# Kernel optimization log

Measured on AMD Instinct MI355X. Metric: run time of the kernel, lower is better.

The kernel has to match this reference:

```python
import jax, jax.numpy as jnp
import numpy as np

N_HEADS = 16
ATT_DIM = 1024
HEAD_DIM = ATT_DIM // N_HEADS
SCALE = 1.0 / (HEAD_DIM ** 0.5)


def setup_inputs() -> dict:
    key = jax.random.key(0)
    k1, k2 = jax.random.split(key)
    B, N, D = 4, 2048, 1024
    X = jax.random.normal(k1, (B, N, D), dtype=jnp.float32)
    W_qkv = jax.random.normal(k2, (3 * ATT_DIM, D), dtype=jnp.float32) * 0.02  # trunc_normal-ish std
    return {"X": X, "W_qkv": W_qkv}


def reference(X, W_qkv):
    B, N, D = X.shape
    # qkv projection (bias=False): X @ W^T -> [b, n, 3*att_dim]
    QKV = jnp.einsum('bnd,od->bno', X, W_qkv)
    # rearrange 'b n (p h d) -> p b h n d'
    QKV = QKV.reshape(B, N, 3, N_HEADS, HEAD_DIM).transpose(2, 0, 3, 1, 4)
    Q, K, V = QKV[0], QKV[1], QKV[2]
    # scaled dot-product attention, full NxN scores (as in source)
    scores = jnp.einsum('bhid,bhjd->bhij', Q, K) * SCALE
    S = jax.nn.softmax(scores, axis=-1)
    # dropout rate is 0.0 -> identity
    Y = jnp.einsum('bhij,bhjd->bhid', S, V)
    # 'b h n d -> b n (h d)'; out_proj is Identity (out_dim == att_dim)
    return Y.transpose(0, 2, 1, 3).reshape(B, N, N_HEADS * HEAD_DIM)
```

## Files before the change

### kernel.cpp

```cpp
#include <hip/hip_runtime.h>

#define BATCH   4
#define SEQ     2048
#define DMODEL  1024
#define NHEADS  16
#define HDIM    64
#define QSC     0.18033688f

typedef short s16x8 __attribute__((ext_vector_type(8)));
typedef float f32x4 __attribute__((ext_vector_type(4)));
typedef const __attribute__((address_space(1))) unsigned int* gas_t;
typedef __attribute__((address_space(3))) unsigned int* las_t;

__device__ inline unsigned short f2bf(float f) {
    unsigned int u = __float_as_uint(f);
    u += 0x7FFF + ((u >> 16) & 1);
    return (unsigned short)(u >> 16);
}

__device__ __forceinline__ float exp2_fast(float x) {
#if __has_builtin(__builtin_amdgcn_exp2f)
    return __builtin_amdgcn_exp2f(x);
#else
    return exp2f(x);
#endif
}

__device__ __forceinline__ float rcp_fast(float x) {
#if __has_builtin(__builtin_amdgcn_rcpf)
    return __builtin_amdgcn_rcpf(x);
#else
    return 1.0f / x;
#endif
}

__device__ __forceinline__ unsigned int pack_bf16x2(float lo, float hi) {
    unsigned int a = __float_as_uint(lo) + 0x8000u;
    unsigned int b = __float_as_uint(hi) + 0x8000u;
#if __has_builtin(__builtin_amdgcn_perm)
    return __builtin_amdgcn_perm(b, a, 0x07060302u);
#else
    return (a >> 16) | (b & 0xFFFF0000u);
#endif
}

__global__ void cvt_bf16(const float* __restrict__ in,
                         unsigned short* __restrict__ out, int n4) {
    int i = blockIdx.x * blockDim.x + threadIdx.x;
    if (i >= n4) return;
    float4 v = ((const float4*)in)[i];
    ushort4 o;
    o.x = f2bf(v.x); o.y = f2bf(v.y); o.z = f2bf(v.z); o.w = f2bf(v.w);
    ((ushort4*)out)[i] = o;
}

__global__ __launch_bounds__(256, 4) void qkv_gemm(
    const unsigned short* __restrict__ Xb,
    const unsigned short* __restrict__ Wb,
    unsigned short* __restrict__ Qo,
    unsigned short* __restrict__ Ko,
    unsigned short* __restrict__ Vt)
{
    __shared__ __align__(16) unsigned short As[2][128 * 32];
    __shared__ __align__(16) unsigned short Bs[2][128 * 32];

    const int t    = threadIdx.x;
    const int m0   = blockIdx.y * 128;
    const int n0   = blockIdx.x * 128;
    const int wid  = t >> 6;
    const int lane = t & 63;
    const int l15  = lane & 15;
    const int quad = lane >> 4;
    const int wm   = (wid >> 1) * 64;
    const int wn   = (wid & 1) * 64;

    const int srow = t >> 1;
    const int koff = (t & 1) * 16;

    const unsigned short* gA = &Xb[(size_t)(m0 + srow) * 1024 + koff];
    const unsigned short* gB = &Wb[(size_t)(n0 + srow) * 1024 + koff];

    f32x4 acc[4][4] = {};
    uint4 ra0, ra1, rb0, rb1;

    auto gload = [&](int k0) {
        const uint4* pa = (const uint4*)(gA + k0);
        ra0 = pa[0]; ra1 = pa[1];
        const uint4* pb = (const uint4*)(gB + k0);
        rb0 = pb[0]; rb1 = pb[1];
    };
    auto swrite = [&](int buf) {
        uint4* sa = (uint4*)&As[buf][srow * 32 + koff];
        sa[0] = ra0; sa[1] = ra1;
        uint4* sb = (uint4*)&Bs[buf][srow * 32 + koff];
        sb[0] = rb0; sb[1] = rb1;
    };

    gload(0);
    swrite(0);
    __syncthreads();

    int cur = 0;
    #pragma unroll 1
    for (int k0 = 0; k0 < 1024; k0 += 32) {
        const bool more = (k0 + 32) < 1024;
        if (more) gload(k0 + 32);

        s16x8 af[4], bf[4];
        #pragma unroll
        for (int mt = 0; mt < 4; mt++)
            af[mt] = *(const s16x8*)&As[cur][(wm + mt * 16 + l15) * 32 + quad * 8];
        #pragma unroll
        for (int nt = 0; nt < 4; nt++)
            bf[nt] = *(const s16x8*)&Bs[cur][(wn + nt * 16 + l15) * 32 + quad * 8];
        #pragma unroll
        for (int mt = 0; mt < 4; mt++)
            #pragma unroll
            for (int nt = 0; nt < 4; nt++)
                acc[mt][nt] = __builtin_amdgcn_mfma_f32_16x16x32_bf16(
                    af[mt], bf[nt], acc[mt][nt], 0, 0, 0);

        if (more) swrite(cur ^ 1);
        __syncthreads();
        cur ^= 1;
    }

    #pragma unroll
    for (int mt = 0; mt < 4; mt++) {
        const int mbase = m0 + wm + mt * 16 + quad * 4;
        #pragma unroll
        for (int nt = 0; nt < 4; nt++) {
            const int o  = n0 + wn + nt * 16 + l15;
            const int p  = o >> 10;
            const int oo = o & 1023;
            const int h  = oo >> 6;
            const int d  = oo & 63;
            #pragma unroll
            for (int r = 0; r < 4; r++) {
                const int mm = mbase + r;
                const int b  = mm >> 11;
                const int n  = mm & 2047;
                float v = acc[mt][nt][r];
                if (p == 0)
                    Qo[((size_t)(b * 16 + h) * 2048 + n) * 64 + d] = f2bf(v * QSC);
                else if (p == 1)
                    Ko[((size_t)(b * 16 + h) * 2048 + n) * 64 + d] = f2bf(v);
                else
                    Vt[((size_t)(b * 16 + h) * 64 + d) * 2048 + n] = f2bf(v);
            }
        }
    }
}

#define PSTRIDE 72
#define PBASE   8192

__global__ __launch_bounds__(256, 4) void attn(
    const unsigned short* __restrict__ Q,
    const unsigned short* __restrict__ K,
    const unsigned short* __restrict__ Vt,
    float* __restrict__ out)
{
    __shared__ __align__(16) unsigned short LDS[PBASE + 4 * 32 * PSTRIDE];

    const int t    = threadIdx.x;
    const int w    = t >> 6;
    const int lane = t & 63;
    const int l15  = lane & 15;
    const int quad = lane >> 4;
    const int head = blockIdx.y;
    const int b    = head >> 4;
    const int h    = head & 15;
    const int q0   = blockIdx.x * 128 + w * 32;

    const unsigned short* Qh = Q  + (size_t)head * 2048 * 64;
    const unsigned short* Kh = K  + (size_t)head * 2048 * 64;
    const unsigned short* Vh = Vt + (size_t)head * 64 * 2048;

    const int r0 = t >> 3;
    const int c0 = (t & 7) ^ (r0 & 7);
    const unsigned short* srcK = Kh + r0 * 64 + c0 * 8;
    const unsigned short* srcV = Vh + r0 * 2048 + c0 * 8;

    auto stage = [&](int kt) {
        #pragma unroll
        for (int rd = 0; rd < 2; rd++) {
            __builtin_amdgcn_global_load_lds(
                (gas_t)(const void*)(srcK + kt * 4096 + rd * 2048),
                (las_t)(void*)&LDS[rd * 2048 + w * 512], 16, 0, 0);
            __builtin_amdgcn_global_load_lds(
                (gas_t)(const void*)(srcV + kt * 64 + rd * 65536),
                (las_t)(void*)&LDS[4096 + rd * 2048 + w * 512], 16, 0, 0);
        }
    };

    s16x8 qb[2][2];
    #pragma unroll
    for (int mt = 0; mt < 2; mt++)
        #pragma unroll
        for (int kc = 0; kc < 2; kc++)
            qb[mt][kc] = *(const s16x8*)&Qh[(size_t)(q0 + mt * 16 + l15) * 64 + kc * 32 + quad * 8];

    f32x4 y[2][4] = {};
    float lsum[2] = {0.f, 0.f};
    unsigned short* P = &LDS[PBASE + w * (32 * PSTRIDE)];

    const int x7   = l15 & 7;
    const int csw0 = (quad ^ x7) * 8;
    const int csw1 = ((4 + quad) ^ x7) * 8;

    stage(0);
    __syncthreads();

    #pragma unroll 1
    for (int kt = 0; kt < 32; kt++) {
        s16x8 kb[4][2];
        #pragma unroll
        for (int nt = 0; nt < 4; nt++) {
            const int rowb = (nt * 16 + l15) * 64;
            kb[nt][0] = *(const s16x8*)&LDS[rowb + csw0];
            kb[nt][1] = *(const s16x8*)&LDS[rowb + csw1];
        }
        f32x4 st[4][2] = {};
        #pragma unroll
        for (int kc = 0; kc < 2; kc++)
            #pragma unroll
            for (int nt = 0; nt < 4; nt++)
                #pragma unroll
                for (int mt = 0; mt < 2; mt++)
                    st[nt][mt] = __builtin_amdgcn_mfma_f32_16x16x32_bf16(
                        kb[nt][kc], qb[mt][kc], st[nt][mt], 0, 0, 0);

        s16x8 vb[4][2];
        #pragma unroll
        for (int dt = 0; dt < 4; dt++) {
            const int rowb = 4096 + (dt * 16 + l15) * 64;
            vb[dt][0] = *(const s16x8*)&LDS[rowb + csw0];
            vb[dt][1] = *(const s16x8*)&LDS[rowb + csw1];
        }

        __syncthreads();
        if (kt + 1 < 32) stage(kt + 1);

        #pragma unroll
        for (int mt = 0; mt < 2; mt++)
            #pragma unroll
            for (int nt = 0; nt < 4; nt++) {
                float p0 = exp2_fast(st[nt][mt][0]);
                float p1 = exp2_fast(st[nt][mt][1]);
                float p2 = exp2_fast(st[nt][mt][2]);
                float p3 = exp2_fast(st[nt][mt][3]);
                lsum[mt] += (p0 + p1) + (p2 + p3);
                uint2 u;
                u.x = pack_bf16x2(p0, p1);
                u.y = pack_bf16x2(p2, p3);
                *(uint2*)&P[(mt * 16 + l15) * PSTRIDE + nt * 16 + quad * 4] = u;
            }
        #pragma unroll
        for (int kc = 0; kc < 2; kc++) {
            s16x8 pa[2];
            #pragma unroll
            for (int mt = 0; mt < 2; mt++)
                pa[mt] = *(const s16x8*)&P[(mt * 16 + l15) * PSTRIDE + kc * 32 + quad * 8];
            #pragma unroll
            for (int mt = 0; mt < 2; mt++)
                #pragma unroll
                for (int dt = 0; dt < 4; dt++)
                    y[mt][dt] = __builtin_amdgcn_mfma_f32_16x16x32_bf16(
                        pa[mt], vb[dt][kc], y[mt][dt], 0, 0, 0);
        }

        __syncthreads();
    }

    #pragma unroll
    for (int mt = 0; mt < 2; mt++) {
        float v = lsum[mt];
        v += __shfl_xor(v, 16);
        v += __shfl_xor(v, 32);
        lsum[mt] = v;
    }

    float rinv[2][4];
    #pragma unroll
    for (int mt = 0; mt < 2; mt++)
        #pragma unroll
        for (int r = 0; r < 4; r++)
            rinv[mt][r] = rcp_fast(__shfl(lsum[mt], quad * 4 + r));

    #pragma unroll
    for (int mt = 0; mt < 2; mt++)
        #pragma unroll
        for (int dt = 0; dt < 4; dt++)
            #pragma unroll
            for (int r = 0; r < 4; r++) {
                const int n = q0 + mt * 16 + quad * 4 + r;
                const int d = dt * 16 + l15;
                out[((size_t)(b * 2048 + n)) * 1024 + h * 64 + d] =
                    y[mt][dt][r] * rinv[mt][r];
            }
}

extern "C" void kernel_launch(void* const* d_in, const int* in_sizes, int n_in,
                              void* d_out, int out_size, void* d_ws, size_t ws_size,
                              hipStream_t stream) {
    const float* X = (const float*)d_in[0];
    const float* W = (const float*)d_in[1];
    float* out = (float*)d_out;

    char* ws = (char*)d_ws;
    unsigned short* Xb = (unsigned short*)(ws);
    unsigned short* Wb = (unsigned short*)(ws + 16777216);
    unsigned short* Qb = (unsigned short*)(ws + 23068672);
    unsigned short* Kb = (unsigned short*)(ws + 39845888);
    unsigned short* Vt = (unsigned short*)(ws + 56623104);

    cvt_bf16<<<dim3(8192), dim3(256), 0, stream>>>(X, Xb, 2097152);
    cvt_bf16<<<dim3(3072), dim3(256), 0, stream>>>(W, Wb, 786432);
    qkv_gemm<<<dim3(24, 64), dim3(256), 0, stream>>>(Xb, Wb, Qb, Kb, Vt);
    attn<<<dim3(16, 64), dim3(256), 0, stream>>>(Qb, Kb, Vt, out);
}
```

Measured before the change: 266.3 us.

## Fuse fp32-to-bf16 conversion into GEMM and double-buffer attention K/V tiles

The separate X and W conversion kernels are removed. The QKV GEMM now loads fp32 directly, packs it to bf16 while writing LDS with a padded stride, and prefetches two k-steps ahead. The attention kernel doubles the query rows per wave to 64 and double-buffers the K/V LDS tiles so the next tile's async load overlaps compute, which removes one barrier per iteration. This trades extra launches and global traffic for more registers and LDS per block, with occupancy lowered to 2 blocks per SIMD bound.

```diff
diff --git a/kernel.cpp b/kernel.cpp
--- a/kernel.cpp
+++ b/kernel.cpp
@@ -44,25 +44,17 @@
 #endif
 }
 
-__global__ void cvt_bf16(const float* __restrict__ in,
-                         unsigned short* __restrict__ out, int n4) {
-    int i = blockIdx.x * blockDim.x + threadIdx.x;
-    if (i >= n4) return;
-    float4 v = ((const float4*)in)[i];
-    ushort4 o;
-    o.x = f2bf(v.x); o.y = f2bf(v.y); o.z = f2bf(v.z); o.w = f2bf(v.w);
-    ((ushort4*)out)[i] = o;
-}
-
-__global__ __launch_bounds__(256, 4) void qkv_gemm(
-    const unsigned short* __restrict__ Xb,
-    const unsigned short* __restrict__ Wb,
+#define GSTR 40
+
+__global__ __launch_bounds__(256, 2) void qkv_gemm(
+    const float* __restrict__ X,
+    const float* __restrict__ W,
     unsigned short* __restrict__ Qo,
     unsigned short* __restrict__ Ko,
     unsigned short* __restrict__ Vt)
 {
-    __shared__ __align__(16) unsigned short As[2][128 * 32];
-    __shared__ __align__(16) unsigned short Bs[2][128 * 32];
+    __shared__ __align__(16) unsigned short As[2][128 * GSTR];
+    __shared__ __align__(16) unsigned short Bs[2][128 * GSTR];
 
     const int t    = threadIdx.x;
     const int m0   = blockIdx.y * 128;
@@ -77,52 +69,64 @@
     const int srow = t >> 1;
     const int koff = (t & 1) * 16;
 
-    const unsigned short* gA = &Xb[(size_t)(m0 + srow) * 1024 + koff];
-    const unsigned short* gB = &Wb[(size_t)(n0 + srow) * 1024 + koff];
+    const float* gA = &X[(size_t)(m0 + srow) * 1024 + koff];
+    const float* gB = &W[(size_t)(n0 + srow) * 1024 + koff];
 
     f32x4 acc[4][4] = {};
-    uint4 ra0, ra1, rb0, rb1;
-
-    auto gload = [&](int k0) {
-        const uint4* pa = (const uint4*)(gA + k0);
-        ra0 = pa[0]; ra1 = pa[1];
-        const uint4* pb = (const uint4*)(gB + k0);
-        rb0 = pb[0]; rb1 = pb[1];
+    float4 sa0[4], sb0[4], sa1[4], sb1[4];
+
+    auto gloadf = [&](int k0, float4 (&a)[4], float4 (&b)[4]) {
+        const float4* pa = (const float4*)(gA + k0);
+        a[0] = pa[0]; a[1] = pa[1]; a[2] = pa[2]; a[3] = pa[3];
+        const float4* pb = (const float4*)(gB + k0);
+        b[0] = pb[0]; b[1] = pb[1]; b[2] = pb[2]; b[3] = pb[3];
     };
-    auto swrite = [&](int buf) {
-        uint4* sa = (uint4*)&As[buf][srow * 32 + koff];
-        sa[0] = ra0; sa[1] = ra1;
-        uint4* sb = (uint4*)&Bs[buf][srow * 32 + koff];
-        sb[0] = rb0; sb[1] = rb1;
+    auto swrite = [&](int buf, float4 (&a)[4], float4 (&b)[4]) {
+        uint4 u;
+        u.x = pack_bf16x2(a[0].x, a[0].y); u.y = pack_bf16x2(a[0].z, a[0].w);
+        u.z = pack_bf16x2(a[1].x, a[1].y); u.w = pack_bf16x2(a[1].z, a[1].w);
+        *(uint4*)&As[buf][srow * GSTR + koff] = u;
+        u.x = pack_bf16x2(a[2].x, a[2].y); u.y = pack_bf16x2(a[2].z, a[2].w);
+        u.z = pack_bf16x2(a[3].x, a[3].y); u.w = pack_bf16x2(a[3].z, a[3].w);
+        *(uint4*)&As[buf][srow * GSTR + koff + 8] = u;
+        u.x = pack_bf16x2(b[0].x, b[0].y); u.y = pack_bf16x2(b[0].z, b[0].w);
+        u.z = pack_bf16x2(b[1].x, b[1].y); u.w = pack_bf16x2(b[1].z, b[1].w);
+        *(uint4*)&Bs[buf][srow * GSTR + koff] = u;
+        u.x = pack_bf16x2(b[2].x, b[2].y); u.y = pack_bf16x2(b[2].z, b[2].w);
+        u.z = pack_bf16x2(b[3].x, b[3].y); u.w = pack_bf16x2(b[3].z, b[3].w);
+        *(uint4*)&Bs[buf][srow * GSTR + koff + 8] = u;
     };
-
-    gload(0);
-    swrite(0);
-    __syncthreads();
-
-    int cur = 0;
-    #pragma unroll 1
-    for (int k0 = 0; k0 < 1024; k0 += 32) {
-        const bool more = (k0 + 32) < 1024;
-        if (more) gload(k0 + 32);
-
+    auto cstep = [&](int buf) {
         s16x8 af[4], bf[4];
         #pragma unroll
         for (int mt = 0; mt < 4; mt++)
-            af[mt] = *(const s16x8*)&As[cur][(wm + mt * 16 + l15) * 32 + quad * 8];
+            af[mt] = *(const s16x8*)&As[buf][(wm + mt * 16 + l15) * GSTR + quad * 8];
         #pragma unroll
         for (int nt = 0; nt < 4; nt++)
-            bf[nt] = *(const s16x8*)&Bs[cur][(wn + nt * 16 + l15) * 32 + quad * 8];
+            bf[nt] = *(const s16x8*)&Bs[buf][(wn + nt * 16 + l15) * GSTR + quad * 8];
         #pragma unroll
         for (int mt = 0; mt < 4; mt++)
             #pragma unroll
             for (int nt = 0; nt < 4; nt++)
                 acc[mt][nt] = __builtin_amdgcn_mfma_f32_16x16x32_bf16(
                     af[mt], bf[nt], acc[mt][nt], 0, 0, 0);
-
-        if (more) swrite(cur ^ 1);
+    };
+
+    gloadf(0, sa0, sb0);
+    swrite(0, sa0, sb0);
+    gloadf(32, sa1, sb1);
+    __syncthreads();
+
+    #pragma unroll 1
+    for (int kk = 0; kk < 1024; kk += 64) {
+        if (kk + 64 < 1024) gloadf(kk + 64, sa0, sb0);
+        cstep(0);
+        swrite(1, sa1, sb1);
         __syncthreads();
-        cur ^= 1;
+        if (kk + 96 < 1024) gloadf(kk + 96, sa1, sb1);
+        cstep(1);
+        if (kk + 64 < 1024) swrite(0, sa0, sb0);
+        __syncthreads();
     }
 
     #pragma unroll
@@ -153,15 +157,15 @@
 }
 
 #define PSTRIDE 72
-#define PBASE   8192
-
-__global__ __launch_bounds__(256, 4) void attn(
+#define PBASE   16384
+
+__global__ __launch_bounds__(256, 2) void attn(
     const unsigned short* __restrict__ Q,
     const unsigned short* __restrict__ K,
     const unsigned short* __restrict__ Vt,
     float* __restrict__ out)
 {
-    __shared__ __align__(16) unsigned short LDS[PBASE + 4 * 32 * PSTRIDE];
+    __shared__ __align__(16) unsigned short LDS[PBASE + 4 * 64 * PSTRIDE];
 
     const int t    = threadIdx.x;
     const int w    = t >> 6;
@@ -171,7 +175,7 @@
     const int head = blockIdx.y;
     const int b    = head >> 4;
     const int h    = head & 15;
-    const int q0   = blockIdx.x * 128 + w * 32;
+    const int q0   = blockIdx.x * 256 + w * 64;
 
     const unsigned short* Qh = Q  + (size_t)head * 2048 * 64;
     const unsigned short* Kh = K  + (size_t)head * 2048 * 64;
@@ -182,68 +186,68 @@
     const unsigned short* srcK = Kh + r0 * 64 + c0 * 8;
     const unsigned short* srcV = Vh + r0 * 2048 + c0 * 8;
 
-    auto stage = [&](int kt) {
+    auto stage = [&](int kt, int bufE) {
         #pragma unroll
         for (int rd = 0; rd < 2; rd++) {
             __builtin_amdgcn_global_load_lds(
                 (gas_t)(const void*)(srcK + kt * 4096 + rd * 2048),
-                (las_t)(void*)&LDS[rd * 2048 + w * 512], 16, 0, 0);
+                (las_t)(void*)&LDS[bufE + rd * 2048 + w * 512], 16, 0, 0);
             __builtin_amdgcn_global_load_lds(
                 (gas_t)(const void*)(srcV + kt * 64 + rd * 65536),
-                (las_t)(void*)&LDS[4096 + rd * 2048 + w * 512], 16, 0, 0);
+                (las_t)(void*)&LDS[bufE + 4096 + rd * 2048 + w * 512], 16, 0, 0);
         }
     };
 
-    s16x8 qb[2][2];
-    #pragma unroll
-    for (int mt = 0; mt < 2; mt++)
+    s16x8 qb[4][2];
+    #pragma unroll
+    for (int mt = 0; mt < 4; mt++)
         #pragma unroll
         for (int kc = 0; kc < 2; kc++)
             qb[mt][kc] = *(const s16x8*)&Qh[(size_t)(q0 + mt * 16 + l15) * 64 + kc * 32 + quad * 8];
 
-    f32x4 y[2][4] = {};
-    float lsum[2] = {0.f, 0.f};
-    unsigned short* P = &LDS[PBASE + w * (32 * PSTRIDE)];
+    f32x4 y[4][4] = {};
+    float lsum[4] = {0.f, 0.f, 0.f, 0.f};
+    unsigned short* P = &LDS[PBASE + w * (64 * PSTRIDE)];
 
     const int x7   = l15 & 7;
     const int csw0 = (quad ^ x7) * 8;
     const int csw1 = ((4 + quad) ^ x7) * 8;
 
-    stage(0);
+    stage(0, 0);
     __syncthreads();
 
     #pragma unroll 1
     for (int kt = 0; kt < 32; kt++) {
+        const int bufE = (kt & 1) * 8192;
+        if (kt + 1 < 32) stage(kt + 1, 8192 - bufE);
+
         s16x8 kb[4][2];
         #pragma unroll
         for (int nt = 0; nt < 4; nt++) {
-            const int rowb = (nt * 16 + l15) * 64;
+            const int rowb = bufE + (nt * 16 + l15) * 64;
             kb[nt][0] = *(const s16x8*)&LDS[rowb + csw0];
             kb[nt][1] = *(const s16x8*)&LDS[rowb + csw1];
         }
-        f32x4 st[4][2] = {};
+        f32x4 st[4][4] = {};
         #pragma unroll
         for (int kc = 0; kc < 2; kc++)
             #pragma unroll
             for (int nt = 0; nt < 4; nt++)
                 #pragma unroll
-                for (int mt = 0; mt < 2; mt++)
+                for (int mt = 0; mt < 4; mt++)
                     st[nt][mt] = __builtin_amdgcn_mfma_f32_16x16x32_bf16(
                         kb[nt][kc], qb[mt][kc], st[nt][mt], 0, 0, 0);
 
         s16x8 vb[4][2];
         #pragma unroll
         for (int dt = 0; dt < 4; dt++) {
-            const int rowb = 4096 + (dt * 16 + l15) * 64;
+            const int rowb = bufE + 4096 + (dt * 16 + l15) * 64;
             vb[dt][0] = *(const s16x8*)&LDS[rowb + csw0];
             vb[dt][1] = *(const s16x8*)&LDS[rowb + csw1];
         }
 
-        __syncthreads();
-        if (kt + 1 < 32) stage(kt + 1);
-
-        #pragma unroll
-        for (int mt = 0; mt < 2; mt++)
+        #pragma unroll
+        for (int mt = 0; mt < 4; mt++)
             #pragma unroll
             for (int nt = 0; nt < 4; nt++) {
                 float p0 = exp2_fast(st[nt][mt][0]);
@@ -256,14 +260,15 @@
                 u.y = pack_bf16x2(p2, p3);
                 *(uint2*)&P[(mt * 16 + l15) * PSTRIDE + nt * 16 + quad * 4] = u;
             }
+
         #pragma unroll
         for (int kc = 0; kc < 2; kc++) {
-            s16x8 pa[2];
-            #pragma unroll
-            for (int mt = 0; mt < 2; mt++)
+            s16x8 pa[4];
+            #pragma unroll
+            for (int mt = 0; mt < 4; mt++)
                 pa[mt] = *(const s16x8*)&P[(mt * 16 + l15) * PSTRIDE + kc * 32 + quad * 8];
             #pragma unroll
-            for (int mt = 0; mt < 2; mt++)
+            for (int mt = 0; mt < 4; mt++)
                 #pragma unroll
                 for (int dt = 0; dt < 4; dt++)
                     y[mt][dt] = __builtin_amdgcn_mfma_f32_16x16x32_bf16(
@@ -274,22 +279,22 @@
     }
 
     #pragma unroll
-    for (int mt = 0; mt < 2; mt++) {
+    for (int mt = 0; mt < 4; mt++) {
         float v = lsum[mt];
         v += __shfl_xor(v, 16);
         v += __shfl_xor(v, 32);
         lsum[mt] = v;
     }
 
-    float rinv[2][4];
-    #pragma unroll
-    for (int mt = 0; mt < 2; mt++)
+    float rinv[4][4];
+    #pragma unroll
+    for (int mt = 0; mt < 4; mt++)
         #pragma unroll
         for (int r = 0; r < 4; r++)
             rinv[mt][r] = rcp_fast(__shfl(lsum[mt], quad * 4 + r));
 
     #pragma unroll
-    for (int mt = 0; mt < 2; mt++)
+    for (int mt = 0; mt < 4; mt++)
         #pragma unroll
         for (int dt = 0; dt < 4; dt++)
             #pragma unroll
@@ -309,14 +314,10 @@
     float* out = (float*)d_out;
 
     char* ws = (char*)d_ws;
-    unsigned short* Xb = (unsigned short*)(ws);
-    unsigned short* Wb = (unsigned short*)(ws + 16777216);
-    unsigned short* Qb = (unsigned short*)(ws + 23068672);
-    unsigned short* Kb = (unsigned short*)(ws + 39845888);
-    unsigned short* Vt = (unsigned short*)(ws + 56623104);
-
-    cvt_bf16<<<dim3(8192), dim3(256), 0, stream>>>(X, Xb, 2097152);
-    cvt_bf16<<<dim3(3072), dim3(256), 0, stream>>>(W, Wb, 786432);
-    qkv_gemm<<<dim3(24, 64), dim3(256), 0, stream>>>(Xb, Wb, Qb, Kb, Vt);
-    attn<<<dim3(16, 64), dim3(256), 0, stream>>>(Qb, Kb, Vt, out);
-}
+    unsigned short* Qb = (unsigned short*)(ws);
+    unsigned short* Kb = (unsigned short*)(ws + 16777216);
+    unsigned short* Vt = (unsigned short*)(ws + 33554432);
+
+    qkv_gemm<<<dim3(24, 64), dim3(256), 0, stream>>>(X, W, Qb, Kb, Vt);
+    attn<<<dim3(8, 64), dim3(256), 0, stream>>>(Qb, Kb, Vt, out);
+}
```

Result: slower. 289.2 us (+8.6%).
